# Optimization experiments

Hardware: AMD Instinct MI355X
Metric: run time of the kernel (lower is better)

Reference implementation:

```python
import jax, jax.numpy as jnp
import numpy as np

N = 50000      # nodes
E = 800000     # edges
INIT = 256     # input feature dim
HID = 64       # per-head hidden dim
EMB = 128      # output embed dim
H = 8          # heads
ALPHA = 0.2    # leaky-relu slope
EPS = 1e-16    # guard for isolated nodes


def setup_inputs() -> dict:
    key = jax.random.key(0)
    ks = jax.random.split(key, 6)
    x = jax.random.normal(ks[0], (N, INIT), dtype=jnp.float32)
    edge_index = jax.random.randint(ks[1], (2, E), 0, N, dtype=jnp.int32)
    # xavier-ish scaling keeps exp(-leakyrelu(.)) in a sane range
    W1 = jax.random.normal(ks[2], (H, INIT, HID), dtype=jnp.float32) / np.sqrt(INIT).astype(np.float32)
    a1 = jax.random.normal(ks[3], (H, 2 * HID), dtype=jnp.float32) / np.sqrt(2 * HID).astype(np.float32)
    Wo = jax.random.normal(ks[4], (H * HID, EMB), dtype=jnp.float32) / np.sqrt(H * HID).astype(np.float32)
    ao = jax.random.normal(ks[5], (2 * EMB,), dtype=jnp.float32) / np.sqrt(2 * EMB).astype(np.float32)
    return {"x": x, "edge_index": edge_index, "W1": W1, "a1": a1, "Wo": Wo, "ao": ao}


def _sp_att_head(x, W, a, src, dst):
    """One sparse GAT head (pyGAT SpGraphAttentionLayer math)."""
    h = x @ W                                              # [N, F']
    eh = jnp.concatenate([h[src], h[dst]], axis=1)          # [E, 2F']
    ee = jnp.exp(-jax.nn.leaky_relu(eh @ a, ALPHA))         # [E]
    denom = jax.ops.segment_sum(ee, src, num_segments=N) + EPS          # [N]
    num = jax.ops.segment_sum(ee[:, None] * h[dst], src, num_segments=N)  # [N, F']
    h_prime = num / denom[:, None]
    att = ee / denom[src]
    return h_prime, att


def reference(x, edge_index, W1, a1, Wo, ao, args=0):
    src, dst = edge_index[0], edge_index[1]
    # first (and only) multi-head layer, concat=True -> elu per head, concat on feature dim
    heads = [jax.nn.elu(_sp_att_head(x, W1[i], a1[i], src, dst)[0]) for i in range(H)]
    x1 = jnp.concatenate(heads, axis=1)                     # [N, H*HID]
    # output attention layer, concat=False; top-level applies elu
    h_prime, att_out = _sp_att_head(x1, Wo, ao, src, dst)
    return jax.nn.elu(h_prime), edge_index, att_out
```

## Files before the change

kernel.cpp:

```cpp
#include <hip/hip_runtime.h>
#include <hip/hip_bf16.h>
#include <cstddef>

#define NN    50000
#define NE    800000
#define FIN   256
#define HID   64
#define NH    8
#define F1    512
#define EMB   128
#define ALPHA 0.2f
#define EPSF  1e-16f
#define NBLK  ((NN + 255) / 256)

#if defined(__has_builtin)
# if __has_builtin(__builtin_amdgcn_cvt_scalef32_pk_f32_fp4) && __has_builtin(__builtin_amdgcn_cvt_scalef32_pk_fp4_f32)
#  define HAVE_FP4 1
# else
#  define HAVE_FP4 0
# endif
#else
# define HAVE_FP4 0
#endif

typedef __hip_bfloat16 bf16;
typedef __attribute__((ext_vector_type(8))) short short8;
typedef __attribute__((ext_vector_type(4))) float f32x4;
typedef __attribute__((ext_vector_type(2))) float f32x2;

#if HAVE_FP4
typedef uint2 pay_t;
#define PAYB1 (F1 / 2)
#define PAYB2 (EMB / 2)
#define SINV1 2.0f
#define SINV2 4.0f
#define PSC1  0.5f
#define PSC2  0.25f
#else
typedef uint4 pay_t;
#define PAYB1 F1
#define PAYB2 EMB
#define SINV1 1.0f
#define SINV2 1.0f
#define PSC1  1.0f
#define PSC2  1.0f
#endif

__device__ __forceinline__ float eluf(float x){ return x > 0.f ? x : __expf(x) - 1.f; }
__device__ __forceinline__ float lrelu_neg_exp(float s){
    float lr = s > 0.f ? s : ALPHA * s;
    return __expf(-lr);
}
__device__ __forceinline__ float b2f(unsigned u){ return __uint_as_float(u << 16); }

__device__ __forceinline__ void fma16pk(f32x2* acc, pay_t q, float e){
    f32x2 e2; e2[0] = e; e2[1] = e;
#if HAVE_FP4
    acc[0] += __builtin_amdgcn_cvt_scalef32_pk_f32_fp4(q.x, 1.0f, 0) * e2;
    acc[1] += __builtin_amdgcn_cvt_scalef32_pk_f32_fp4(q.x, 1.0f, 1) * e2;
    acc[2] += __builtin_amdgcn_cvt_scalef32_pk_f32_fp4(q.x, 1.0f, 2) * e2;
    acc[3] += __builtin_amdgcn_cvt_scalef32_pk_f32_fp4(q.x, 1.0f, 3) * e2;
    acc[4] += __builtin_amdgcn_cvt_scalef32_pk_f32_fp4(q.y, 1.0f, 0) * e2;
    acc[5] += __builtin_amdgcn_cvt_scalef32_pk_f32_fp4(q.y, 1.0f, 1) * e2;
    acc[6] += __builtin_amdgcn_cvt_scalef32_pk_f32_fp4(q.y, 1.0f, 2) * e2;
    acc[7] += __builtin_amdgcn_cvt_scalef32_pk_f32_fp4(q.y, 1.0f, 3) * e2;
#else
    acc[0] += __builtin_amdgcn_cvt_pk_f32_fp8(q.x, false) * e2;
    acc[1] += __builtin_amdgcn_cvt_pk_f32_fp8(q.x, true)  * e2;
    acc[2] += __builtin_amdgcn_cvt_pk_f32_fp8(q.y, false) * e2;
    acc[3] += __builtin_amdgcn_cvt_pk_f32_fp8(q.y, true)  * e2;
    acc[4] += __builtin_amdgcn_cvt_pk_f32_fp8(q.z, false) * e2;
    acc[5] += __builtin_amdgcn_cvt_pk_f32_fp8(q.z, true)  * e2;
    acc[6] += __builtin_amdgcn_cvt_pk_f32_fp8(q.w, false) * e2;
    acc[7] += __builtin_amdgcn_cvt_pk_f32_fp8(q.w, true)  * e2;
#endif
}

__device__ __forceinline__ unsigned bpack(float a, float b){
    unsigned ua = __float_as_uint(a), ub = __float_as_uint(b);
    ua = (ua + 0x7fffu + ((ua >> 16) & 1)) >> 16;
    ub = (ub + 0x7fffu + ((ub >> 16) & 1)) >> 16;
    return (ua & 0xffffu) | (ub << 16);
}

__global__ void k_tw1(const float* __restrict__ W1, bf16* __restrict__ Bt1){
    int i = blockIdx.x * 256 + threadIdx.x;
    if (i >= F1 * FIN) return;
    int n = i >> 8, k = i & 255;
    Bt1[i] = __float2bfloat16(W1[(size_t)(n >> 6) * FIN * HID + (size_t)k * HID + (n & 63)]);
}

__global__ void k_tw2(const float* __restrict__ Wo, bf16* __restrict__ WoT){
    int i = blockIdx.x * 256 + threadIdx.x;
    if (i >= EMB * F1) return;
    int n = i >> 9, k = i & 511;
    WoT[i] = __float2bfloat16(Wo[(size_t)k * EMB + n]);
}

__global__ void k_q4(const unsigned char* __restrict__ in, unsigned* __restrict__ out,
                     int n8, float sinv){
    int i = blockIdx.x * 256 + threadIdx.x;
    if (i >= n8) return;
    uint2 v = *(const uint2*)(in + (size_t)i * 8);
#if HAVE_FP4
    f32x2 a = __builtin_amdgcn_cvt_pk_f32_fp8(v.x, false);
    f32x2 b = __builtin_amdgcn_cvt_pk_f32_fp8(v.x, true);
    f32x2 c = __builtin_amdgcn_cvt_pk_f32_fp8(v.y, false);
    f32x2 d = __builtin_amdgcn_cvt_pk_f32_fp8(v.y, true);
    unsigned r = 0;
    r = __builtin_amdgcn_cvt_scalef32_pk_fp4_f32(r, a[0] * sinv, a[1] * sinv, 1.0f, 0);
    r = __builtin_amdgcn_cvt_scalef32_pk_fp4_f32(r, b[0] * sinv, b[1] * sinv, 1.0f, 1);
    r = __builtin_amdgcn_cvt_scalef32_pk_fp4_f32(r, c[0] * sinv, c[1] * sinv, 1.0f, 2);
    r = __builtin_amdgcn_cvt_scalef32_pk_fp4_f32(r, d[0] * sinv, d[1] * sinv, 1.0f, 3);
    out[i] = r;
#else
    (void)sinv;
    *(uint2*)((unsigned char*)out + (size_t)i * 8) = v;
#endif
}

__global__ void k_zero(int* p, int n){
    int i = blockIdx.x * 256 + threadIdx.x;
    if (i < n) p[i] = 0;
}

__global__ void k_count(const int* __restrict__ src, int* __restrict__ cnt){
    int e = blockIdx.x * 256 + threadIdx.x;
    if (e < NE) atomicAdd(&cnt[src[e]], 1);
}

__global__ __launch_bounds__(256) void k_bsum(const int* __restrict__ cnt, int* __restrict__ bsum){
    const int b = blockIdx.x, t = threadIdx.x, idx = b * 256 + t;
    int v = (idx < NN) ? cnt[idx] : 0;
#pragma unroll
    for (int o = 1; o < 64; o <<= 1) v += __shfl_xor(v, o);
    __shared__ int ws[4];
    if ((t & 63) == 0) ws[t >> 6] = v;
    __syncthreads();
    if (t == 0) bsum[b] = ws[0] + ws[1] + ws[2] + ws[3];
}

__global__ __launch_bounds__(256) void k_scanb(const int* __restrict__ bsum,
                                               int* __restrict__ boff,
                                               int* __restrict__ rp){
    const int t = threadIdx.x;
    __shared__ int s[256];
    const int v = (t < NBLK) ? bsum[t] : 0;
    s[t] = v;
    __syncthreads();
    for (int o = 1; o < 256; o <<= 1){
        int u = (t >= o) ? s[t - o] : 0;
        __syncthreads();
        s[t] += u;
        __syncthreads();
    }
    if (t < NBLK) boff[t] = s[t] - v;
    if (t == 255) rp[NN] = s[255];
}

__global__ __launch_bounds__(256) void k_rp(const int* __restrict__ cnt,
                                            const int* __restrict__ boff,
                                            int* __restrict__ rp){
    const int b = blockIdx.x, t = threadIdx.x, idx = b * 256 + t;
    const int v = (idx < NN) ? cnt[idx] : 0;
    __shared__ int s[256];
    s[t] = v;
    __syncthreads();
    for (int o = 1; o < 256; o <<= 1){
        int u = (t >= o) ? s[t - o] : 0;
        __syncthreads();
        s[t] += u;
        __syncthreads();
    }
    if (idx < NN) rp[idx] = boff[b] + s[t] - v;
}

__global__ void k_scatter(const int* __restrict__ src, const int* __restrict__ dst,
                          const int* __restrict__ rp, int* __restrict__ cur,
                          int* __restrict__ sdst, int* __restrict__ ssrc){
    int e = blockIdx.x * 256 + threadIdx.x;
    if (e < NE){
        int s = src[e];
        int p = atomicAdd(&cur[s], 1);
        sdst[rp[s] + p] = dst[e];
        ssrc[rp[s] + p] = s;
    }
}

__global__ void k_ee(const int* __restrict__ ssrc, const int* __restrict__ sdst,
                     const float* __restrict__ s11, const float* __restrict__ s12,
                     unsigned short* __restrict__ ee8b){
    int i = blockIdx.x * 256 + threadIdx.x;
    if (i >= NE) return;
    int s = ssrc[i], d = sdst[i];
    const float* ps = s11 + (size_t)s * NH;
    const float* pd = s12 + (size_t)d * NH;
    float e[8];
#pragma unroll
    for (int h = 0; h < 8; h++) e[h] = lrelu_neg_exp(ps[h] + pd[h]);
    uint4 o;
    o.x = bpack(e[0], e[1]); o.y = bpack(e[2], e[3]);
    o.z = bpack(e[4], e[5]); o.w = bpack(e[6], e[7]);
    *(uint4*)(ee8b + (size_t)i * 8) = o;
}

__global__ __launch_bounds__(256) void k_gemm1f(const float* __restrict__ A,
                                                const bf16* __restrict__ B,
                                                unsigned char* __restrict__ C){
    constexpr int K = FIN, N = F1;
    constexpr int LDT = 40;
    __shared__ __align__(16) bf16 As[128 * LDT];
    __shared__ __align__(16) bf16 Bs[128 * LDT];
    const int t = threadIdx.x;
    const int lane = t & 63, wid = t >> 6;
    const int m0 = blockIdx.x * 128, n0 = blockIdx.y * 128;
    const int r0 = t >> 2, u0 = t & 3;
    const int r1 = r0 + 64;
    const int rb = (wid & 1) * 64, cb = (wid >> 1) * 64;
    const int fr = lane & 15, fk = (lane >> 4) * 8;

    f32x4 acc[4][4];
#pragma unroll
    for (int i = 0; i < 4; i++)
#pragma unroll
        for (int j = 0; j < 4; j++) acc[i][j] = (f32x4)(0.f);

    for (int k0 = 0; k0 < K; k0 += 32){
        const int ga0 = m0 + r0, ga1 = m0 + r1;
        float4 a0a = make_float4(0,0,0,0), a0b = a0a, a1a = a0a, a1b = a0a;
        if (ga0 < NN){
            const float* p = A + (size_t)ga0 * K + k0 + u0 * 8;
            a0a = *(const float4*)p; a0b = *(const float4*)(p + 4);
        }
        if (ga1 < NN){
            const float* p = A + (size_t)ga1 * K + k0 + u0 * 8;
            a1a = *(const float4*)p; a1b = *(const float4*)(p + 4);
        }
        uint4 av0, av1;
        av0.x = bpack(a0a.x, a0a.y); av0.y = bpack(a0a.z, a0a.w);
        av0.z = bpack(a0b.x, a0b.y); av0.w = bpack(a0b.z, a0b.w);
        av1.x = bpack(a1a.x, a1a.y); av1.y = bpack(a1a.z, a1a.w);
        av1.z = bpack(a1b.x, a1b.y); av1.w = bpack(a1b.z, a1b.w);
        uint4 bv0 = *(const uint4*)(B + (size_t)(n0 + r0) * K + k0 + u0 * 8);
        uint4 bv1 = *(const uint4*)(B + (size_t)(n0 + r1) * K + k0 + u0 * 8);
        __syncthreads();
        *(uint4*)(As + r0 * LDT + u0 * 8) = av0;
        *(uint4*)(As + r1 * LDT + u0 * 8) = av1;
        *(uint4*)(Bs + r0 * LDT + u0 * 8) = bv0;
        *(uint4*)(Bs + r1 * LDT + u0 * 8) = bv1;
        __syncthreads();
        short8 af[4], bf_[4];
#pragma unroll
        for (int i = 0; i < 4; i++){
            af[i]  = *(const short8*)(As + (rb + i * 16 + fr) * LDT + fk);
            bf_[i] = *(const short8*)(Bs + (cb + i * 16 + fr) * LDT + fk);
        }
#pragma unroll
        for (int i = 0; i < 4; i++)
#pragma unroll
            for (int j = 0; j < 4; j++)
                acc[i][j] = __builtin_amdgcn_mfma_f32_16x16x32_bf16(af[i], bf_[j], acc[i][j], 0, 0, 0);
    }
    const int crow = m0 + rb + (lane >> 4) * 4;
    const int ccol = n0 + cb + (lane & 15);
#pragma unroll
    for (int i = 0; i < 4; i++)
#pragma unroll
        for (int j = 0; j < 4; j++)
#pragma unroll
            for (int v = 0; v < 4; v++){
                int row = crow + i * 16 + v;
                if (row < NN){
                    float val = acc[i][j][v];
                    unsigned r = __builtin_amdgcn_cvt_pk_fp8_f32(val, val, 0u, false);
                    C[(size_t)row * N + ccol + j * 16] = (unsigned char)(r & 0xffu);
                }
            }
}

template<int K>
__global__ __launch_bounds__(256) void k_mgemm(const bf16* __restrict__ A,
                                               const bf16* __restrict__ B,
                                               unsigned char* __restrict__ C,
                                               int N){
    constexpr int LDT = 40;
    __shared__ __align__(16) bf16 As[128 * LDT];
    __shared__ __align__(16) bf16 Bs[128 * LDT];
    const int t = threadIdx.x;
    const int lane = t & 63, wid = t >> 6;
    const int m0 = blockIdx.x * 128, n0 = blockIdx.y * 128;
    const int r0 = t >> 2, u0 = t & 3;
    const int r1 = r0 + 64;
    const int rb = (wid & 1) * 64, cb = (wid >> 1) * 64;
    const int fr = lane & 15, fk = (lane >> 4) * 8;

    f32x4 acc[4][4];
#pragma unroll
    for (int i = 0; i < 4; i++)
#pragma unroll
        for (int j = 0; j < 4; j++) acc[i][j] = (f32x4)(0.f);

    for (int k0 = 0; k0 < K; k0 += 32){
        const int ga0 = m0 + r0, ga1 = m0 + r1;
        uint4 av0 = (ga0 < NN) ? *(const uint4*)(A + (size_t)ga0 * K + k0 + u0 * 8)
                               : make_uint4(0, 0, 0, 0);
        uint4 av1 = (ga1 < NN) ? *(const uint4*)(A + (size_t)ga1 * K + k0 + u0 * 8)
                               : make_uint4(0, 0, 0, 0);
        uint4 bv0 = *(const uint4*)(B + (size_t)(n0 + r0) * K + k0 + u0 * 8);
        uint4 bv1 = *(const uint4*)(B + (size_t)(n0 + r1) * K + k0 + u0 * 8);
        __syncthreads();
        *(uint4*)(As + r0 * LDT + u0 * 8) = av0;
        *(uint4*)(As + r1 * LDT + u0 * 8) = av1;
        *(uint4*)(Bs + r0 * LDT + u0 * 8) = bv0;
        *(uint4*)(Bs + r1 * LDT + u0 * 8) = bv1;
        __syncthreads();
        short8 af[4], bf_[4];
#pragma unroll
        for (int i = 0; i < 4; i++){
            af[i]  = *(const short8*)(As + (rb + i * 16 + fr) * LDT + fk);
            bf_[i] = *(const short8*)(Bs + (cb + i * 16 + fr) * LDT + fk);
        }
#pragma unroll
        for (int i = 0; i < 4; i++)
#pragma unroll
            for (int j = 0; j < 4; j++)
                acc[i][j] = __builtin_amdgcn_mfma_f32_16x16x32_bf16(af[i], bf_[j], acc[i][j], 0, 0, 0);
    }
    const int crow = m0 + rb + (lane >> 4) * 4;
    const int ccol = n0 + cb + (lane & 15);
#pragma unroll
    for (int i = 0; i < 4; i++)
#pragma unroll
        for (int j = 0; j < 4; j++)
#pragma unroll
            for (int v = 0; v < 4; v++){
                int row = crow + i * 16 + v;
                if (row < NN){
                    float val = acc[i][j][v];
                    unsigned r = __builtin_amdgcn_cvt_pk_fp8_f32(val, val, 0u, false);
                    C[(size_t)row * N + ccol + j * 16] = (unsigned char)(r & 0xffu);
                }
            }
}

__global__ void k_s1q(const unsigned char* __restrict__ h1q, const float* __restrict__ a1,
                      float* __restrict__ s11, float* __restrict__ s12,
                      unsigned char* __restrict__ pay){
    int idx = blockIdx.x * 256 + threadIdx.x;
    if (idx >= NN * NH) return;
    int n = idx >> 3, h = idx & 7;
    const uint4* hp = (const uint4*)(h1q + (size_t)n * F1 + h * HID);
    const float* a  = a1 + (size_t)h * 2 * HID;
    float d1 = 0.f, d2 = 0.f;
    float f[64];
#pragma unroll
    for (int u = 0; u < 4; u++){
        uint4 q = hp[u];
        int j = u * 16;
        f32x2 p;
        p = __builtin_amdgcn_cvt_pk_f32_fp8(q.x, false); f[j+0]=p[0];  f[j+1]=p[1];
        p = __builtin_amdgcn_cvt_pk_f32_fp8(q.x, true);  f[j+2]=p[0];  f[j+3]=p[1];
        p = __builtin_amdgcn_cvt_pk_f32_fp8(q.y, false); f[j+4]=p[0];  f[j+5]=p[1];
        p = __builtin_amdgcn_cvt_pk_f32_fp8(q.y, true);  f[j+6]=p[0];  f[j+7]=p[1];
        p = __builtin_amdgcn_cvt_pk_f32_fp8(q.z, false); f[j+8]=p[0];  f[j+9]=p[1];
        p = __builtin_amdgcn_cvt_pk_f32_fp8(q.z, true);  f[j+10]=p[0]; f[j+11]=p[1];
        p = __builtin_amdgcn_cvt_pk_f32_fp8(q.w, false); f[j+12]=p[0]; f[j+13]=p[1];
        p = __builtin_amdgcn_cvt_pk_f32_fp8(q.w, true);  f[j+14]=p[0]; f[j+15]=p[1];
    }
#pragma unroll
    for (int j = 0; j < 64; j++){
        d1 += f[j] * a[j];
        d2 += f[j] * a[HID + j];
    }
    s11[idx] = d1;
    s12[idx] = d2;
#if HAVE_FP4
    unsigned w8[8];
#pragma unroll
    for (int u = 0; u < 8; u++){
        unsigned rr = 0;
        int j = u * 8;
        rr = __builtin_amdgcn_cvt_scalef32_pk_fp4_f32(rr, f[j+0]*SINV1, f[j+1]*SINV1, 1.0f, 0);
        rr = __builtin_amdgcn_cvt_scalef32_pk_fp4_f32(rr, f[j+2]*SINV1, f[j+3]*SINV1, 1.0f, 1);
        rr = __builtin_amdgcn_cvt_scalef32_pk_fp4_f32(rr, f[j+4]*SINV1, f[j+5]*SINV1, 1.0f, 2);
        rr = __builtin_amdgcn_cvt_scalef32_pk_fp4_f32(rr, f[j+6]*SINV1, f[j+7]*SINV1, 1.0f, 3);
        w8[u] = rr;
    }
    uint4* op = (uint4*)(pay + (size_t)n * PAYB1 + h * (HID / 2));
    uint4 o0, o1;
    o0.x = w8[0]; o0.y = w8[1]; o0.z = w8[2]; o0.w = w8[3];
    o1.x = w8[4]; o1.y = w8[5]; o1.z = w8[6]; o1.w = w8[7];
    op[0] = o0; op[1] = o1;
#else
    uint4* op = (uint4*)(pay + (size_t)n * PAYB1 + h * HID);
    op[0] = hp[0]; op[1] = hp[1]; op[2] = hp[2]; op[3] = hp[3];
#endif
}

__global__ __launch_bounds__(256) void k_agg1(const unsigned char* __restrict__ hq,
                                              const unsigned short* __restrict__ ee8b,
                                              const int* __restrict__ rp,
                                              const int* __restrict__ sdst,
                                              bf16* __restrict__ x1){
    const int t = threadIdx.x, lane = t & 63, w = t >> 6;
    const int n = blockIdx.x * 4 + w;
    const int l32 = lane & 31;
    const int half = lane >> 5;
    const int hf = l32 >> 2;
    const int eslot = lane >> 3;
    f32x2 acc[8];
#pragma unroll
    for (int i = 0; i < 8; i++){ acc[i][0] = 0.f; acc[i][1] = 0.f; }
    float dedp = 0.f;
    const int start = rp[n], end = rp[n + 1];
    const unsigned char* __restrict__ hl = hq + (size_t)l32 * (PAYB1 / 32);
    for (int c0 = start; c0 < end; c0 += 64){
        const int m = min(64, end - c0);
        int dreg = (lane < m) ? sdst[c0 + lane] : 0;
        for (int g = 0; g * 8 < m; g++){
            unsigned short eu = ee8b[(size_t)(c0 + g * 8) * 8 + lane];
            dedp += (g * 8 + eslot < m) ? b2f(eu) : 0.f;
        }
        for (int j = 0; j < m; j += 16){
            int dj[8]; unsigned short eu[8]; pay_t q[8];
#pragma unroll
            for (int p = 0; p < 8; p++){
                const int e2 = j + 2 * p + half;
                dj[p] = __shfl(dreg, e2);
                eu[p] = ee8b[(size_t)(c0 + e2) * 8 + hf];
                q[p]  = *(const pay_t*)(hl + (size_t)dj[p] * PAYB1);
            }
#pragma unroll
            for (int p = 0; p < 8; p++){
                const int e2 = j + 2 * p + half;
                const float e = (e2 < m) ? b2f(eu[p]) : 0.f;
                fma16pk(acc, q[p], e);
            }
        }
    }
    dedp += __shfl_xor(dedp, 8);
    dedp += __shfl_xor(dedp, 16);
    dedp += __shfl_xor(dedp, 32);
#pragma unroll
    for (int i = 0; i < 8; i++){
        acc[i][0] += __shfl_xor(acc[i][0], 32);
        acc[i][1] += __shfl_xor(acc[i][1], 32);
    }
    float ded = __shfl(dedp, hf);
    const float inv = PSC1 / (ded + EPSF);
    if (half == 0){
        float o[16];
#pragma unroll
        for (int i = 0; i < 8; i++){
            o[2 * i]     = eluf(acc[i][0] * inv);
            o[2 * i + 1] = eluf(acc[i][1] * inv);
        }
        uint4 ov0, ov1;
        ov0.x = bpack(o[0], o[1]);   ov0.y = bpack(o[2], o[3]);
        ov0.z = bpack(o[4], o[5]);   ov0.w = bpack(o[6], o[7]);
        ov1.x = bpack(o[8], o[9]);   ov1.y = bpack(o[10], o[11]);
        ov1.z = bpack(o[12], o[13]); ov1.w = bpack(o[14], o[15]);
        bf16* xp = x1 + (size_t)n * F1 + l32 * 16;
        *(uint4*)xp = ov0;
        *(uint4*)(xp + 8) = ov1;
    }
}

__global__ void k_s2(const unsigned char* __restrict__ h2q, const float* __restrict__ ao,
                     float* __restrict__ s21, float* __restrict__ s22){
    int n = blockIdx.x * 256 + threadIdx.x;
    if (n >= NN) return;
    const uint4* hp = (const uint4*)(h2q + (size_t)n * EMB);
    float d1 = 0.f, d2 = 0.f;
#pragma unroll
    for (int u = 0; u < 8; u++){
        uint4 q = hp[u];
        int j = u * 16;
#define S2(w, o) { f32x2 p0 = __builtin_amdgcn_cvt_pk_f32_fp8((w), false); \
                   f32x2 p1 = __builtin_amdgcn_cvt_pk_f32_fp8((w), true); \
                   d1 += p0[0]*ao[(o)] + p0[1]*ao[(o)+1] + p1[0]*ao[(o)+2] + p1[1]*ao[(o)+3]; \
                   d2 += p0[0]*ao[EMB+(o)] + p0[1]*ao[EMB+(o)+1] + p1[0]*ao[EMB+(o)+2] + p1[1]*ao[EMB+(o)+3]; }
        S2(q.x, j) S2(q.y, j + 4) S2(q.z, j + 8) S2(q.w, j + 12)
#undef S2
    }
    s21[n] = d1;
    s22[n] = d2;
}

__global__ __launch_bounds__(256) void k_agg2(const unsigned char* __restrict__ hq,
                                              const float* __restrict__ s21,
                                              const float* __restrict__ s22,
                                              const int* __restrict__ rp,
                                              const int* __restrict__ sdst,
                                              float* __restrict__ den2,
                                              float* __restrict__ out0){
    const int t = threadIdx.x, lane = t & 63, w = t >> 6;
    const int n = blockIdx.x * 4 + w;
    const int slot = lane >> 3;
    const int fpos = lane & 7;
    const float s1v = s21[n];
    f32x2 acc[8];
#pragma unroll
    for (int i = 0; i < 8; i++){ acc[i][0] = 0.f; acc[i][1] = 0.f; }
    float dedp = 0.f;
    const int start = rp[n], end = rp[n + 1];
    const unsigned char* __restrict__ hl = hq + (size_t)fpos * (PAYB2 / 8);
    for (int c0 = start; c0 < end; c0 += 64){
        const int m = min(64, end - c0);
        int dreg = (lane < m) ? sdst[c0 + lane] : 0;
        float ev = (lane < m) ? lrelu_neg_exp(s1v + s22[dreg]) : 0.f;
        dedp += ev;
        for (int j = 0; j < m; j += 8){
            const int ei = j + slot;
            const float e = __shfl(ev, ei);
            const int   d = __shfl(dreg, ei);
            pay_t q = *(const pay_t*)(hl + (size_t)d * PAYB2);
            fma16pk(acc, q, e);
        }
    }
#pragma unroll
    for (int o = 1; o <= 32; o <<= 1) dedp += __shfl_xor(dedp, o);
#pragma unroll
    for (int o = 8; o <= 32; o <<= 1)
#pragma unroll
        for (int i = 0; i < 8; i++){
            acc[i][0] += __shfl_xor(acc[i][0], o);
            acc[i][1] += __shfl_xor(acc[i][1], o);
        }
    const float den = dedp + EPSF;
    if (slot == 0){
        const float inv = PSC2 / den;
        float* op = out0 + (size_t)n * EMB + fpos * 16;
#pragma unroll
        for (int u = 0; u < 4; u++){
            float4 ov;
            ov.x = eluf(acc[2 * u][0] * inv);
            ov.y = eluf(acc[2 * u][1] * inv);
            ov.z = eluf(acc[2 * u + 1][0] * inv);
            ov.w = eluf(acc[2 * u + 1][1] * inv);
            *(float4*)(op + u * 4) = ov;
        }
        if (lane == 0) den2[n] = den;
    }
}

__global__ void k_att_edge(const int* __restrict__ ei,
                           const float* __restrict__ s21, const float* __restrict__ s22,
                           const float* __restrict__ den2,
                           float* __restrict__ outE, float* __restrict__ outA){
    int i = blockIdx.x * 256 + threadIdx.x;
    if (i < 2 * NE) outE[i] = (float)ei[i];
    if (i < NE){
        int s = ei[i], d = ei[NE + i];
        float ee = lrelu_neg_exp(s21[s] + s22[d]);
        outA[i] = ee / den2[s];
    }
}

extern "C" void kernel_launch(void* const* d_in, const int* in_sizes, int n_in,
                              void* d_out, int out_size, void* d_ws, size_t ws_size,
                              hipStream_t stream){
    const float* x  = (const float*)d_in[0];
    const int*   ei = (const int*)d_in[1];
    const float* W1 = (const float*)d_in[2];
    const float* a1 = (const float*)d_in[3];
    const float* Wo = (const float*)d_in[4];
    const float* ao = (const float*)d_in[5];
    float* out = (float*)d_out;
    const int* src = ei;
    const int* dst = ei + NE;

    char* w = (char*)d_ws;
    auto alloc = [&](size_t bytes) -> char* {
        char* p = w;
        w += (bytes + 255) & ~(size_t)255;
        return p;
    };
    unsigned char* h1pay = (unsigned char*)alloc((size_t)NN * F1);
    bf16*  x1   = (bf16*) alloc((size_t)NN * F1 * 2);
    unsigned char* h1q = (unsigned char*)alloc((size_t)NN * F1);
    unsigned char* h2q = (unsigned char*)alloc((size_t)NN * EMB);
    unsigned short* ee8b = (unsigned short*)alloc(((size_t)NE + 64) * 8 * 2);
    bf16*  Bt1  = (bf16*) alloc((size_t)F1 * FIN * 2);
    bf16*  WoT  = (bf16*) alloc((size_t)EMB * F1 * 2);
    float* s11  = (float*)alloc((size_t)NN * NH * 4);
    float* s12  = (float*)alloc((size_t)NN * NH * 4);
    float* s21  = (float*)alloc((size_t)NN * 4);
    float* s22  = (float*)alloc((size_t)NN * 4);
    float* den2 = (float*)alloc((size_t)NN * 4);
    int*   cnt2 = (int*)  alloc((size_t)2 * NN * 4);
    int*   rp   = (int*)  alloc((size_t)(NN + 1) * 4);
    int*   sdst = (int*)  alloc((size_t)NE * 4);
    int*   ssrc = (int*)  alloc((size_t)NE * 4);
    int*   bsum = (int*)  alloc((size_t)NBLK * 4);
    int*   boff = (int*)  alloc((size_t)NBLK * 4);
    int*   cnt = cnt2;
    int*   cur = cnt2 + NN;
    unsigned char* h2pay = (unsigned char*)x1;

    k_tw1<<<(F1 * FIN + 255) / 256, 256, 0, stream>>>(W1, Bt1);
    k_tw2<<<(EMB * F1 + 255) / 256, 256, 0, stream>>>(Wo, WoT);

    k_zero   <<<(2 * NN + 255) / 256, 256, 0, stream>>>(cnt2, 2 * NN);
    k_count  <<<(NE + 255) / 256,     256, 0, stream>>>(src, cnt);
    k_bsum   <<<NBLK,                 256, 0, stream>>>(cnt, bsum);
    k_scanb  <<<1,                    256, 0, stream>>>(bsum, boff, rp);
    k_rp     <<<NBLK,                 256, 0, stream>>>(cnt, boff, rp);
    k_scatter<<<(NE + 255) / 256,     256, 0, stream>>>(src, dst, rp, cur, sdst, ssrc);

    k_gemm1f<<<dim3((NN + 127) / 128, F1 / 128), 256, 0, stream>>>(x, Bt1, h1q);
    k_s1q <<<(NN * NH + 255) / 256, 256, 0, stream>>>(h1q, a1, s11, s12, h1pay);
    k_ee  <<<(NE + 255) / 256, 256, 0, stream>>>(ssrc, sdst, s11, s12, ee8b);
    k_agg1<<<NN / 4, 256, 0, stream>>>(h1pay, ee8b, rp, sdst, x1);

    k_mgemm<F1><<<dim3((NN + 127) / 128, EMB / 128), 256, 0, stream>>>(x1, WoT, h2q, EMB);
    k_q4  <<<(NN * EMB / 8 + 255) / 256, 256, 0, stream>>>(h2q, (unsigned*)h2pay, NN * EMB / 8, SINV2);
    k_s2  <<<(NN + 255) / 256, 256, 0, stream>>>(h2q, ao, s21, s22);
    k_agg2<<<NN / 4, 256, 0, stream>>>(h2pay, s21, s22, rp, sdst, den2, out);

    k_att_edge<<<(2 * NE + 255) / 256, 256, 0, stream>>>(ei, s21, s22, den2,
                                                         out + (size_t)NN * EMB,
                                                         out + (size_t)NN * EMB + 2 * NE);
}
```

Measured before the change: 335.8 us.

## Fuse edge scatter with layer-1 scores, precompute layer-2 edge weights, retile GEMM2

Merges the CSR scatter with the layer-1 per-edge exp-score computation, so each edge's weights are computed once and written directly at their sorted position. This removes a separate pass over the sorted edge arrays. Adds a k_ee2 kernel that precomputes layer-2 edge weights so k_agg2 reads them instead of gathering s22 and evaluating exp inline. Also replaces the generic 128x128 GEMM2 with a 64-row tile over the full 128-column output, interleaves FP4 packing into the fp8 score loop in k_s1q, and vectorizes the attention/edge output kernel with int4/float4. The trade-offs are an extra kernel launch and NE*4 bytes of workspace, and gemm1/s1q now sit between the rowptr scan and the scatter.

```diff
diff --git a/kernel.cpp b/kernel.cpp
--- a/kernel.cpp
+++ b/kernel.cpp
@@ -175,33 +175,35 @@
     if (idx < NN) rp[idx] = boff[b] + s[t] - v;
 }
 
-__global__ void k_scatter(const int* __restrict__ src, const int* __restrict__ dst,
-                          const int* __restrict__ rp, int* __restrict__ cur,
-                          int* __restrict__ sdst, int* __restrict__ ssrc){
+__global__ void k_scatter_ee(const int* __restrict__ src, const int* __restrict__ dst,
+                             const int* __restrict__ rp, int* __restrict__ cur,
+                             const float* __restrict__ s11, const float* __restrict__ s12,
+                             int* __restrict__ sdst, int* __restrict__ ssrc,
+                             unsigned short* __restrict__ ee8b){
     int e = blockIdx.x * 256 + threadIdx.x;
-    if (e < NE){
-        int s = src[e];
-        int p = atomicAdd(&cur[s], 1);
-        sdst[rp[s] + p] = dst[e];
-        ssrc[rp[s] + p] = s;
-    }
-}
-
-__global__ void k_ee(const int* __restrict__ ssrc, const int* __restrict__ sdst,
-                     const float* __restrict__ s11, const float* __restrict__ s12,
-                     unsigned short* __restrict__ ee8b){
+    if (e >= NE) return;
+    int s = src[e], d = dst[e];
+    int p = atomicAdd(&cur[s], 1);
+    int pos = rp[s] + p;
+    sdst[pos] = d;
+    ssrc[pos] = s;
+    const float* ps = s11 + (size_t)s * NH;
+    const float* pd = s12 + (size_t)d * NH;
+    float w[8];
+#pragma unroll
+    for (int h = 0; h < 8; h++) w[h] = lrelu_neg_exp(ps[h] + pd[h]);
+    uint4 o;
+    o.x = bpack(w[0], w[1]); o.y = bpack(w[2], w[3]);
+    o.z = bpack(w[4], w[5]); o.w = bpack(w[6], w[7]);
+    *(uint4*)(ee8b + (size_t)pos * 8) = o;
+}
+
+__global__ void k_ee2(const int* __restrict__ ssrc, const int* __restrict__ sdst,
+                      const float* __restrict__ s21, const float* __restrict__ s22,
+                      float* __restrict__ ee2){
     int i = blockIdx.x * 256 + threadIdx.x;
     if (i >= NE) return;
-    int s = ssrc[i], d = sdst[i];
-    const float* ps = s11 + (size_t)s * NH;
-    const float* pd = s12 + (size_t)d * NH;
-    float e[8];
-#pragma unroll
-    for (int h = 0; h < 8; h++) e[h] = lrelu_neg_exp(ps[h] + pd[h]);
-    uint4 o;
-    o.x = bpack(e[0], e[1]); o.y = bpack(e[2], e[3]);
-    o.z = bpack(e[4], e[5]); o.w = bpack(e[6], e[7]);
-    *(uint4*)(ee8b + (size_t)i * 8) = o;
+    ee2[i] = lrelu_neg_exp(s21[ssrc[i]] + s22[sdst[i]]);
 }
 
 __global__ __launch_bounds__(256) void k_gemm1f(const float* __restrict__ A,
@@ -278,58 +280,54 @@
             }
 }
 
-template<int K>
-__global__ __launch_bounds__(256) void k_mgemm(const bf16* __restrict__ A,
-                                               const bf16* __restrict__ B,
-                                               unsigned char* __restrict__ C,
-                                               int N){
+__global__ __launch_bounds__(256) void k_gemm2n(const bf16* __restrict__ A,
+                                                const bf16* __restrict__ B,
+                                                unsigned char* __restrict__ C){
+    constexpr int K = F1, N = EMB;
     constexpr int LDT = 40;
-    __shared__ __align__(16) bf16 As[128 * LDT];
+    __shared__ __align__(16) bf16 As[64 * LDT];
     __shared__ __align__(16) bf16 Bs[128 * LDT];
     const int t = threadIdx.x;
     const int lane = t & 63, wid = t >> 6;
-    const int m0 = blockIdx.x * 128, n0 = blockIdx.y * 128;
-    const int r0 = t >> 2, u0 = t & 3;
-    const int r1 = r0 + 64;
-    const int rb = (wid & 1) * 64, cb = (wid >> 1) * 64;
+    const int m0 = blockIdx.x * 64;
+    const int r = t >> 2, u0 = t & 3;
+    const int rb = (wid & 1) * 32, cb = (wid >> 1) * 64;
     const int fr = lane & 15, fk = (lane >> 4) * 8;
 
-    f32x4 acc[4][4];
-#pragma unroll
-    for (int i = 0; i < 4; i++)
+    f32x4 acc[2][4];
+#pragma unroll
+    for (int i = 0; i < 2; i++)
 #pragma unroll
         for (int j = 0; j < 4; j++) acc[i][j] = (f32x4)(0.f);
 
     for (int k0 = 0; k0 < K; k0 += 32){
-        const int ga0 = m0 + r0, ga1 = m0 + r1;
-        uint4 av0 = (ga0 < NN) ? *(const uint4*)(A + (size_t)ga0 * K + k0 + u0 * 8)
-                               : make_uint4(0, 0, 0, 0);
-        uint4 av1 = (ga1 < NN) ? *(const uint4*)(A + (size_t)ga1 * K + k0 + u0 * 8)
-                               : make_uint4(0, 0, 0, 0);
-        uint4 bv0 = *(const uint4*)(B + (size_t)(n0 + r0) * K + k0 + u0 * 8);
-        uint4 bv1 = *(const uint4*)(B + (size_t)(n0 + r1) * K + k0 + u0 * 8);
-        __syncthreads();
-        *(uint4*)(As + r0 * LDT + u0 * 8) = av0;
-        *(uint4*)(As + r1 * LDT + u0 * 8) = av1;
-        *(uint4*)(Bs + r0 * LDT + u0 * 8) = bv0;
-        *(uint4*)(Bs + r1 * LDT + u0 * 8) = bv1;
-        __syncthreads();
-        short8 af[4], bf_[4];
-#pragma unroll
-        for (int i = 0; i < 4; i++){
-            af[i]  = *(const short8*)(As + (rb + i * 16 + fr) * LDT + fk);
-            bf_[i] = *(const short8*)(Bs + (cb + i * 16 + fr) * LDT + fk);
-        }
-#pragma unroll
-        for (int i = 0; i < 4; i++)
+        const int ga = m0 + r;
+        uint4 av = (ga < NN) ? *(const uint4*)(A + (size_t)ga * K + k0 + u0 * 8)
+                             : make_uint4(0, 0, 0, 0);
+        uint4 bv0 = *(const uint4*)(B + (size_t)r * K + k0 + u0 * 8);
+        uint4 bv1 = *(const uint4*)(B + (size_t)(r + 64) * K + k0 + u0 * 8);
+        __syncthreads();
+        *(uint4*)(As + r * LDT + u0 * 8) = av;
+        *(uint4*)(Bs + r * LDT + u0 * 8) = bv0;
+        *(uint4*)(Bs + (r + 64) * LDT + u0 * 8) = bv1;
+        __syncthreads();
+        short8 af[2], bf_[4];
+#pragma unroll
+        for (int i = 0; i < 2; i++)
+            af[i] = *(const short8*)(As + (rb + i * 16 + fr) * LDT + fk);
+#pragma unroll
+        for (int j = 0; j < 4; j++)
+            bf_[j] = *(const short8*)(Bs + (cb + j * 16 + fr) * LDT + fk);
+#pragma unroll
+        for (int i = 0; i < 2; i++)
 #pragma unroll
             for (int j = 0; j < 4; j++)
                 acc[i][j] = __builtin_amdgcn_mfma_f32_16x16x32_bf16(af[i], bf_[j], acc[i][j], 0, 0, 0);
     }
     const int crow = m0 + rb + (lane >> 4) * 4;
-    const int ccol = n0 + cb + (lane & 15);
-#pragma unroll
-    for (int i = 0; i < 4; i++)
+    const int ccol = cb + (lane & 15);
+#pragma unroll
+    for (int i = 0; i < 2; i++)
 #pragma unroll
         for (int j = 0; j < 4; j++)
 #pragma unroll
@@ -337,8 +335,8 @@
                 int row = crow + i * 16 + v;
                 if (row < NN){
                     float val = acc[i][j][v];
-                    unsigned r = __builtin_amdgcn_cvt_pk_fp8_f32(val, val, 0u, false);
-                    C[(size_t)row * N + ccol + j * 16] = (unsigned char)(r & 0xffu);
+                    unsigned r8 = __builtin_amdgcn_cvt_pk_fp8_f32(val, val, 0u, false);
+                    C[(size_t)row * N + ccol + j * 16] = (unsigned char)(r8 & 0xffu);
                 }
             }
 }
@@ -352,40 +350,45 @@
     const uint4* hp = (const uint4*)(h1q + (size_t)n * F1 + h * HID);
     const float* a  = a1 + (size_t)h * 2 * HID;
     float d1 = 0.f, d2 = 0.f;
-    float f[64];
+#if HAVE_FP4
+    unsigned w8[8];
+#endif
 #pragma unroll
     for (int u = 0; u < 4; u++){
         uint4 q = hp[u];
         int j = u * 16;
-        f32x2 p;
-        p = __builtin_amdgcn_cvt_pk_f32_fp8(q.x, false); f[j+0]=p[0];  f[j+1]=p[1];
-        p = __builtin_amdgcn_cvt_pk_f32_fp8(q.x, true);  f[j+2]=p[0];  f[j+3]=p[1];
-        p = __builtin_amdgcn_cvt_pk_f32_fp8(q.y, false); f[j+4]=p[0];  f[j+5]=p[1];
-        p = __builtin_amdgcn_cvt_pk_f32_fp8(q.y, true);  f[j+6]=p[0];  f[j+7]=p[1];
-        p = __builtin_amdgcn_cvt_pk_f32_fp8(q.z, false); f[j+8]=p[0];  f[j+9]=p[1];
-        p = __builtin_amdgcn_cvt_pk_f32_fp8(q.z, true);  f[j+10]=p[0]; f[j+11]=p[1];
-        p = __builtin_amdgcn_cvt_pk_f32_fp8(q.w, false); f[j+12]=p[0]; f[j+13]=p[1];
-        p = __builtin_amdgcn_cvt_pk_f32_fp8(q.w, true);  f[j+14]=p[0]; f[j+15]=p[1];
-    }
-#pragma unroll
-    for (int j = 0; j < 64; j++){
-        d1 += f[j] * a[j];
-        d2 += f[j] * a[HID + j];
+        f32x2 p0 = __builtin_amdgcn_cvt_pk_f32_fp8(q.x, false);
+        f32x2 p1 = __builtin_amdgcn_cvt_pk_f32_fp8(q.x, true);
+        f32x2 p2 = __builtin_amdgcn_cvt_pk_f32_fp8(q.y, false);
+        f32x2 p3 = __builtin_amdgcn_cvt_pk_f32_fp8(q.y, true);
+        f32x2 p4 = __builtin_amdgcn_cvt_pk_f32_fp8(q.z, false);
+        f32x2 p5 = __builtin_amdgcn_cvt_pk_f32_fp8(q.z, true);
+        f32x2 p6 = __builtin_amdgcn_cvt_pk_f32_fp8(q.w, false);
+        f32x2 p7 = __builtin_amdgcn_cvt_pk_f32_fp8(q.w, true);
+        d1 += p0[0]*a[j+0] + p0[1]*a[j+1] + p1[0]*a[j+2] + p1[1]*a[j+3]
+            + p2[0]*a[j+4] + p2[1]*a[j+5] + p3[0]*a[j+6] + p3[1]*a[j+7]
+            + p4[0]*a[j+8] + p4[1]*a[j+9] + p5[0]*a[j+10]+ p5[1]*a[j+11]
+            + p6[0]*a[j+12]+ p6[1]*a[j+13]+ p7[0]*a[j+14]+ p7[1]*a[j+15];
+        d2 += p0[0]*a[HID+j+0] + p0[1]*a[HID+j+1] + p1[0]*a[HID+j+2] + p1[1]*a[HID+j+3]
+            + p2[0]*a[HID+j+4] + p2[1]*a[HID+j+5] + p3[0]*a[HID+j+6] + p3[1]*a[HID+j+7]
+            + p4[0]*a[HID+j+8] + p4[1]*a[HID+j+9] + p5[0]*a[HID+j+10]+ p5[1]*a[HID+j+11]
+            + p6[0]*a[HID+j+12]+ p6[1]*a[HID+j+13]+ p7[0]*a[HID+j+14]+ p7[1]*a[HID+j+15];
+#if HAVE_FP4
+        unsigned r0 = 0, r1 = 0;
+        r0 = __builtin_amdgcn_cvt_scalef32_pk_fp4_f32(r0, p0[0]*SINV1, p0[1]*SINV1, 1.0f, 0);
+        r0 = __builtin_amdgcn_cvt_scalef32_pk_fp4_f32(r0, p1[0]*SINV1, p1[1]*SINV1, 1.0f, 1);
+        r0 = __builtin_amdgcn_cvt_scalef32_pk_fp4_f32(r0, p2[0]*SINV1, p2[1]*SINV1, 1.0f, 2);
+        r0 = __builtin_amdgcn_cvt_scalef32_pk_fp4_f32(r0, p3[0]*SINV1, p3[1]*SINV1, 1.0f, 3);
+        r1 = __builtin_amdgcn_cvt_scalef32_pk_fp4_f32(r1, p4[0]*SINV1, p4[1]*SINV1, 1.0f, 0);
+        r1 = __builtin_amdgcn_cvt_scalef32_pk_fp4_f32(r1, p5[0]*SINV1, p5[1]*SINV1, 1.0f, 1);
+        r1 = __builtin_amdgcn_cvt_scalef32_pk_fp4_f32(r1, p6[0]*SINV1, p6[1]*SINV1, 1.0f, 2);
+        r1 = __builtin_amdgcn_cvt_scalef32_pk_fp4_f32(r1, p7[0]*SINV1, p7[1]*SINV1, 1.0f, 3);
+        w8[2 * u] = r0; w8[2 * u + 1] = r1;
+#endif
     }
     s11[idx] = d1;
     s12[idx] = d2;
 #if HAVE_FP4
-    unsigned w8[8];
-#pragma unroll
-    for (int u = 0; u < 8; u++){
-        unsigned rr = 0;
-        int j = u * 8;
-        rr = __builtin_amdgcn_cvt_scalef32_pk_fp4_f32(rr, f[j+0]*SINV1, f[j+1]*SINV1, 1.0f, 0);
-        rr = __builtin_amdgcn_cvt_scalef32_pk_fp4_f32(rr, f[j+2]*SINV1, f[j+3]*SINV1, 1.0f, 1);
-        rr = __builtin_amdgcn_cvt_scalef32_pk_fp4_f32(rr, f[j+4]*SINV1, f[j+5]*SINV1, 1.0f, 2);
-        rr = __builtin_amdgcn_cvt_scalef32_pk_fp4_f32(rr, f[j+6]*SINV1, f[j+7]*SINV1, 1.0f, 3);
-        w8[u] = rr;
-    }
     uint4* op = (uint4*)(pay + (size_t)n * PAYB1 + h * (HID / 2));
     uint4 o0, o1;
     o0.x = w8[0]; o0.y = w8[1]; o0.z = w8[2]; o0.w = w8[3];
@@ -488,8 +491,7 @@
 }
 
 __global__ __launch_bounds__(256) void k_agg2(const unsigned char* __restrict__ hq,
-                                              const float* __restrict__ s21,
-                                              const float* __restrict__ s22,
+                                              const float* __restrict__ ee2,
                                               const int* __restrict__ rp,
                                               const int* __restrict__ sdst,
                                               float* __restrict__ den2,
@@ -498,7 +500,6 @@
     const int n = blockIdx.x * 4 + w;
     const int slot = lane >> 3;
     const int fpos = lane & 7;
-    const float s1v = s21[n];
     f32x2 acc[8];
 #pragma unroll
     for (int i = 0; i < 8; i++){ acc[i][0] = 0.f; acc[i][1] = 0.f; }
@@ -508,7 +509,7 @@
     for (int c0 = start; c0 < end; c0 += 64){
         const int m = min(64, end - c0);
         int dreg = (lane < m) ? sdst[c0 + lane] : 0;
-        float ev = (lane < m) ? lrelu_neg_exp(s1v + s22[dreg]) : 0.f;
+        float ev = (lane < m) ? ee2[c0 + lane] : 0.f;
         dedp += ev;
         for (int j = 0; j < m; j += 8){
             const int ei = j + slot;
@@ -544,17 +545,24 @@
     }
 }
 
-__global__ void k_att_edge(const int* __restrict__ ei,
-                           const float* __restrict__ s21, const float* __restrict__ s22,
-                           const float* __restrict__ den2,
-                           float* __restrict__ outE, float* __restrict__ outA){
+__global__ void k_att_edge4(const int* __restrict__ ei,
+                            const float* __restrict__ s21, const float* __restrict__ s22,
+                            const float* __restrict__ den2,
+                            float* __restrict__ outE, float* __restrict__ outA){
     int i = blockIdx.x * 256 + threadIdx.x;
-    if (i < 2 * NE) outE[i] = (float)ei[i];
-    if (i < NE){
-        int s = ei[i], d = ei[NE + i];
-        float ee = lrelu_neg_exp(s21[s] + s22[d]);
-        outA[i] = ee / den2[s];
-    }
+    if (i >= NE / 4) return;
+    int4 s4 = ((const int4*)ei)[i];
+    int4 d4 = ((const int4*)(ei + NE))[i];
+    float4 fs = make_float4((float)s4.x, (float)s4.y, (float)s4.z, (float)s4.w);
+    float4 fd = make_float4((float)d4.x, (float)d4.y, (float)d4.z, (float)d4.w);
+    ((float4*)outE)[i] = fs;
+    ((float4*)(outE + NE))[i] = fd;
+    float4 av;
+    av.x = lrelu_neg_exp(s21[s4.x] + s22[d4.x]) / den2[s4.x];
+    av.y = lrelu_neg_exp(s21[s4.y] + s22[d4.y]) / den2[s4.y];
+    av.z = lrelu_neg_exp(s21[s4.z] + s22[d4.z]) / den2[s4.z];
+    av.w = lrelu_neg_exp(s21[s4.w] + s22[d4.w]) / den2[s4.w];
+    ((float4*)outA)[i] = av;
 }
 
 extern "C" void kernel_launch(void* const* d_in, const int* in_sizes, int n_in,
@@ -581,6 +589,7 @@
     unsigned char* h1q = (unsigned char*)alloc((size_t)NN * F1);
     unsigned char* h2q = (unsigned char*)alloc((size_t)NN * EMB);
     unsigned short* ee8b = (unsigned short*)alloc(((size_t)NE + 64) * 8 * 2);
+    float* ee2  = (float*)alloc((size_t)NE * 4);
     bf16*  Bt1  = (bf16*) alloc((size_t)F1 * FIN * 2);
     bf16*  WoT  = (bf16*) alloc((size_t)EMB * F1 * 2);
     float* s11  = (float*)alloc((size_t)NN * NH * 4);
@@ -601,24 +610,25 @@
     k_tw1<<<(F1 * FIN + 255) / 256, 256, 0, stream>>>(W1, Bt1);
     k_tw2<<<(EMB * F1 + 255) / 256, 256, 0, stream>>>(Wo, WoT);
 
-    k_zero   <<<(2 * NN + 255) / 256, 256, 0, stream>>>(cnt2, 2 * NN);
-    k_count  <<<(NE + 255) / 256,     256, 0, stream>>>(src, cnt);
-    k_bsum   <<<NBLK,                 256, 0, stream>>>(cnt, bsum);
-    k_scanb  <<<1,                    256, 0, stream>>>(bsum, boff, rp);
-    k_rp     <<<NBLK,                 256, 0, stream>>>(cnt, boff, rp);
-    k_scatter<<<(NE + 255) / 256,     256, 0, stream>>>(src, dst, rp, cur, sdst, ssrc);
+    k_zero <<<(2 * NN + 255) / 256, 256, 0, stream>>>(cnt2, 2 * NN);
+    k_count<<<(NE + 255) / 256,     256, 0, stream>>>(src, cnt);
+    k_bsum <<<NBLK,                 256, 0, stream>>>(cnt, bsum);
+    k_scanb<<<1,                    256, 0, stream>>>(bsum, boff, rp);
+    k_rp   <<<NBLK,                 256, 0, stream>>>(cnt, boff, rp);
 
     k_gemm1f<<<dim3((NN + 127) / 128, F1 / 128), 256, 0, stream>>>(x, Bt1, h1q);
     k_s1q <<<(NN * NH + 255) / 256, 256, 0, stream>>>(h1q, a1, s11, s12, h1pay);
-    k_ee  <<<(NE + 255) / 256, 256, 0, stream>>>(ssrc, sdst, s11, s12, ee8b);
+    k_scatter_ee<<<(NE + 255) / 256, 256, 0, stream>>>(src, dst, rp, cur, s11, s12,
+                                                       sdst, ssrc, ee8b);
     k_agg1<<<NN / 4, 256, 0, stream>>>(h1pay, ee8b, rp, sdst, x1);
 
-    k_mgemm<F1><<<dim3((NN + 127) / 128, EMB / 128), 256, 0, stream>>>(x1, WoT, h2q, EMB);
+    k_gemm2n<<<(NN + 63) / 64, 256, 0, stream>>>(x1, WoT, h2q);
     k_q4  <<<(NN * EMB / 8 + 255) / 256, 256, 0, stream>>>(h2q, (unsigned*)h2pay, NN * EMB / 8, SINV2);
     k_s2  <<<(NN + 255) / 256, 256, 0, stream>>>(h2q, ao, s21, s22);
-    k_agg2<<<NN / 4, 256, 0, stream>>>(h2pay, s21, s22, rp, sdst, den2, out);
-
-    k_att_edge<<<(2 * NE + 255) / 256, 256, 0, stream>>>(ei, s21, s22, den2,
-                                                         out + (size_t)NN * EMB,
-                                                         out + (size_t)NN * EMB + 2 * NE);
-}
+    k_ee2 <<<(NE + 255) / 256, 256, 0, stream>>>(ssrc, sdst, s21, s22, ee2);
+    k_agg2<<<NN / 4, 256, 0, stream>>>(h2pay, ee2, rp, sdst, den2, out);
+
+    k_att_edge4<<<(NE / 4 + 255) / 256, 256, 0, stream>>>(ei, s21, s22, den2,
+                                                          out + (size_t)NN * EMB,
+                                                          out + (size_t)NN * EMB + 2 * NE);
+}
```

Result: faster. 319.7 us (-4.8%).
